# Performance work log

Measured on AMD Instinct MI355X. Metric: run time of the kernel, lower is better.

Reference implementation:

```python
import jax, jax.numpy as jnp
import numpy as np

N_NODES = 20000
N_EDGES = 320000
IN_DIM = 512
NUM_CLASSES = 10
DROP_P = 0.2


def _gcn_conv(x, src, dst, W, b, n):
    # PyG GCNConv: linear transform, add self-loops, symmetric deg^-1/2 norm,
    # scatter-add into destination nodes, then bias.
    h = x @ W                                   # [N, out]
    loops = jnp.arange(n)
    s = jnp.concatenate([src, loops])           # source (j)
    d = jnp.concatenate([dst, loops])           # destination (i)
    deg = jax.ops.segment_sum(jnp.ones_like(s, dtype=h.dtype), d, num_segments=n)
    dinv = jax.lax.rsqrt(deg)                   # deg >= 1 thanks to self-loops
    norm = dinv[s] * dinv[d]                    # [E+N]
    msg = h[s] * norm[:, None]                  # gather + per-edge scale
    out = jax.ops.segment_sum(msg, d, num_segments=n)  # scatter-add
    return out + b


def _dropout(x, key, p=DROP_P):
    keep = jax.random.bernoulli(key, 1.0 - p, x.shape)
    return jnp.where(keep, x / (1.0 - p), jnp.zeros((), x.dtype))


def setup_inputs() -> dict:
    key = jax.random.key(0)
    ks = jax.random.split(key, 6)
    x = jax.random.normal(ks[0], (N_NODES, IN_DIM), dtype=jnp.float32)
    edge_index = jax.random.randint(ks[1], (2, N_EDGES), 0, N_NODES, dtype=jnp.int64)
    h1, h2 = IN_DIM // 2, IN_DIM // 4
    W1 = jax.random.normal(ks[2], (IN_DIM, h1), dtype=jnp.float32) / np.sqrt(IN_DIM)
    W2 = jax.random.normal(ks[3], (h1, h2), dtype=jnp.float32) / np.sqrt(h1)
    W3 = jax.random.normal(ks[4], (h2, NUM_CLASSES), dtype=jnp.float32) / np.sqrt(h2)
    b1 = jnp.zeros((h1,), jnp.float32)
    b2 = jnp.zeros((h2,), jnp.float32)
    b3 = jnp.zeros((NUM_CLASSES,), jnp.float32)
    return {"x": x, "edge_index": edge_index, "W1": W1, "b1": b1,
            "W2": W2, "b2": b2, "W3": W3, "b3": b3}


def reference(x, edge_index, W1, b1, W2, b2, W3, b3):
    n = x.shape[0]
    src, dst = edge_index[0], edge_index[1]
    dk1, dk2 = jax.random.split(jax.random.key(1))
    h = _gcn_conv(x, src, dst, W1, b1, n)
    h = _dropout(jax.nn.relu(h), dk1)
    h = _gcn_conv(h, src, dst, W2, b2, n)
    h = _dropout(jax.nn.relu(h), dk2)
    h = _gcn_conv(h, src, dst, W3, b3, n)
    return jax.nn.log_softmax(h, axis=1)
```

## Files before the change

kernel.cpp:

```cpp
#include <hip/hip_runtime.h>
#include <hip/hip_bf16.h>
#include <math.h>

typedef __attribute__((ext_vector_type(8))) short short8;
typedef __attribute__((ext_vector_type(8))) unsigned short ushort8;
typedef __attribute__((ext_vector_type(4))) unsigned short ushort4v;
typedef __attribute__((ext_vector_type(4))) float f32x4;

__host__ __device__ inline void threefry2x32(unsigned k0, unsigned k1,
                                             unsigned x0, unsigned x1,
                                             unsigned* out0, unsigned* out1) {
  unsigned ks0 = k0, ks1 = k1, ks2 = k0 ^ k1 ^ 0x1BD11BDAu;
  x0 += ks0; x1 += ks1;
#define TF_ROUND(r) { x0 += x1; x1 = (x1 << (r)) | (x1 >> (32 - (r))); x1 ^= x0; }
  TF_ROUND(13) TF_ROUND(15) TF_ROUND(26) TF_ROUND(6)
  x0 += ks1; x1 += ks2 + 1u;
  TF_ROUND(17) TF_ROUND(29) TF_ROUND(16) TF_ROUND(24)
  x0 += ks2; x1 += ks0 + 2u;
  TF_ROUND(13) TF_ROUND(15) TF_ROUND(26) TF_ROUND(6)
  x0 += ks0; x1 += ks1 + 3u;
  TF_ROUND(17) TF_ROUND(29) TF_ROUND(16) TF_ROUND(24)
  x0 += ks1; x1 += ks2 + 4u;
  TF_ROUND(13) TF_ROUND(15) TF_ROUND(26) TF_ROUND(6)
  x0 += ks2; x1 += ks0 + 5u;
#undef TF_ROUND
  *out0 = x0; *out1 = x1;
}

__device__ inline float jax_uniform01(unsigned key0, unsigned key1, unsigned i) {
  unsigned o0, o1;
  threefry2x32(key0, key1, 0u, i, &o0, &o1);
  unsigned bits = o0 ^ o1;
  return __uint_as_float((bits >> 9) | 0x3f800000u) - 1.0f;
}

__device__ inline unsigned short f2bf(float f) {
  unsigned u = __float_as_uint(f);
  u += 0x7fffu + ((u >> 16) & 1u);
  return (unsigned short)(u >> 16);
}

__device__ inline float bf2f(unsigned short b) {
  return __uint_as_float(((unsigned)b) << 16);
}

__global__ __launch_bounds__(256) void k_init(int* __restrict__ deg, int n,
                                              const float* __restrict__ W1,
                                              unsigned short* __restrict__ W1T,
                                              const float* __restrict__ W2,
                                              unsigned short* __restrict__ W2T) {
  const int S1 = 512 * 256, S2 = 256 * 128;
  int idx = blockIdx.x * 256 + threadIdx.x;
  if (idx < n) { deg[idx] = 0; return; }
  idx -= n;
  if (idx < S1) {
    int k = idx / 256, c = idx % 256;
    W1T[(size_t)c * 512 + k] = f2bf(W1[idx]);
    return;
  }
  idx -= S1;
  if (idx < S2) {
    int k = idx / 128, c = idx % 128;
    W2T[(size_t)c * 256 + k] = f2bf(W2[idx]);
  }
}

__global__ void k_deg(const int* __restrict__ ei, int E, int* __restrict__ deg) {
  int e = blockIdx.x * blockDim.x + threadIdx.x;
  if (e >= E) return;
  atomicAdd(&deg[ei[E + e]], 1);
}

__global__ __launch_bounds__(256) void k_bsum(const int* __restrict__ deg,
                                              int* __restrict__ bsum, int n) {
  int i = blockIdx.x * 256 + threadIdx.x;
  int v = (i < n) ? deg[i] : 0;
#pragma unroll
  for (int o = 32; o; o >>= 1) v += __shfl_down(v, o);
  __shared__ int ws[4];
  if ((threadIdx.x & 63) == 0) ws[threadIdx.x >> 6] = v;
  __syncthreads();
  if (threadIdx.x == 0) bsum[blockIdx.x] = ws[0] + ws[1] + ws[2] + ws[3];
}

__global__ __launch_bounds__(256) void k_scatter2(const int* __restrict__ deg,
                                                  const int* __restrict__ bsum,
                                                  int* __restrict__ off, int* __restrict__ cur,
                                                  float* __restrict__ dinv, int n) {
  int i = blockIdx.x * 256 + threadIdx.x;
  int lane = threadIdx.x & 63, w = threadIdx.x >> 6;
  int pb = 0;
  for (int k = lane; k < blockIdx.x; k += 64) pb += bsum[k];
#pragma unroll
  for (int o = 32; o; o >>= 1) pb += __shfl_xor(pb, o);

  int d = (i < n) ? deg[i] : 0;
  int inc = d;
#pragma unroll
  for (int o = 1; o < 64; o <<= 1) {
    int u = __shfl_up(inc, o);
    if (lane >= o) inc += u;
  }
  __shared__ int wsum[4];
  if (lane == 63) wsum[w] = inc;
  __syncthreads();
  int wbase = 0;
  for (int k = 0; k < w; ++k) wbase += wsum[k];
  int excl = inc - d + wbase + pb;
  if (i < n) {
    off[i] = excl;
    cur[i] = excl;
    dinv[i] = 1.0f / sqrtf((float)(d + 1));
    if (i == n - 1) off[n] = excl + d;
  }
}

__global__ void k_fill_w(const int* __restrict__ ei, int E,
                         int* __restrict__ cur, int* __restrict__ srcs,
                         float* __restrict__ wgt, const float* __restrict__ dinv) {
  int e = blockIdx.x * blockDim.x + threadIdx.x;
  if (e >= E) return;
  int s = ei[e];
  int d = ei[E + e];
  int pos = atomicAdd(&cur[d], 1);
  srcs[pos] = s;
  wgt[pos] = dinv[s] * dinv[d];
}

template <int BN, bool AF32, bool OBF>
__global__ __launch_bounds__(256) void k_gemm_mfma(const void* __restrict__ Ap,
                                                   const unsigned short* __restrict__ BT,
                                                   void* __restrict__ Cp,
                                                   int M, int N, int K) {
  constexpr int WCOLS = BN / 4;
  constexpr int NFW = WCOLS / 16;
  __shared__ unsigned short As[32][40];
  __shared__ unsigned short Bs[BN][40];
  const int tid = threadIdx.x;
  const int row0 = blockIdx.y * 32;
  const int col0 = blockIdx.x * BN;
  const int wn = tid >> 6, lane = tid & 63;
  const int lr = lane & 15, lk = lane >> 4;

  f32x4 acc[2][NFW];
#pragma unroll
  for (int mi = 0; mi < 2; ++mi)
#pragma unroll
    for (int ni = 0; ni < NFW; ++ni) acc[mi][ni] = (f32x4)0.0f;

  const int ar = tid >> 3;
  const int aseg = (tid & 7) * 4;

  for (int k0 = 0; k0 < K; k0 += 32) {
    {
      int grow = row0 + ar;
      unsigned short a4[4] = {0, 0, 0, 0};
      if (grow < M) {
        if (AF32) {
          const float* A = (const float*)Ap;
          float4 v = *(const float4*)&A[(size_t)grow * K + k0 + aseg];
          a4[0] = f2bf(v.x); a4[1] = f2bf(v.y); a4[2] = f2bf(v.z); a4[3] = f2bf(v.w);
        } else {
          const unsigned short* A = (const unsigned short*)Ap;
          ushort4v v = *(const ushort4v*)&A[(size_t)grow * K + k0 + aseg];
          a4[0] = v[0]; a4[1] = v[1]; a4[2] = v[2]; a4[3] = v[3];
        }
      }
      *(ushort4v*)&As[ar][aseg] = *(ushort4v*)a4;
    }
#pragma unroll
    for (int p = 0; p < BN / 64; ++p) {
      int u = tid + p * 256;
      int br = u >> 2;
      int bseg = (u & 3) * 8;
      ushort8 bv = *(const ushort8*)&BT[(size_t)(col0 + br) * K + k0 + bseg];
      *(ushort8*)&Bs[br][bseg] = bv;
    }
    __syncthreads();

    short8 a[2], b[NFW];
#pragma unroll
    for (int mi = 0; mi < 2; ++mi)
      a[mi] = *(const short8*)&As[mi * 16 + lr][lk * 8];
#pragma unroll
    for (int ni = 0; ni < NFW; ++ni)
      b[ni] = *(const short8*)&Bs[wn * WCOLS + ni * 16 + lr][lk * 8];
#pragma unroll
    for (int mi = 0; mi < 2; ++mi)
#pragma unroll
      for (int ni = 0; ni < NFW; ++ni)
        acc[mi][ni] = __builtin_amdgcn_mfma_f32_16x16x32_bf16(a[mi], b[ni], acc[mi][ni], 0, 0, 0);
    __syncthreads();
  }

#pragma unroll
  for (int mi = 0; mi < 2; ++mi) {
    int rbase = row0 + mi * 16 + lk * 4;
#pragma unroll
    for (int j = 0; j < 4; ++j) {
      int row = rbase + j;
      if (row < M) {
#pragma unroll
        for (int ni = 0; ni < NFW; ++ni) {
          int col = col0 + wn * WCOLS + ni * 16 + lr;
          if (OBF) {
            ((unsigned short*)Cp)[(size_t)row * N + col] = f2bf(acc[mi][ni][j]);
          } else {
            ((float*)Cp)[(size_t)row * N + col] = acc[mi][ni][j];
          }
        }
      }
    }
  }
}

template <int C, bool OBF>
__global__ __launch_bounds__(256) void k_agg_bf(const unsigned short* __restrict__ h,
                                                void* __restrict__ outv,
                                                const int* __restrict__ off,
                                                const int* __restrict__ srcs,
                                                const float* __restrict__ wgt,
                                                const float* __restrict__ dinv,
                                                const float* __restrict__ bias,
                                                unsigned key0, unsigned key1, int n) {
  typedef __attribute__((ext_vector_type(C))) unsigned short ushortC;
  const int node = blockIdx.x * (blockDim.x >> 6) + (threadIdx.x >> 6);
  if (node >= n) return;
  const int lane = threadIdx.x & 63;
  const int F = 64 * C;
  const float dv = dinv[node];

  float acc[C];
  {
    ushortC r = *(const ushortC*)(h + (size_t)node * F + lane * C);
    float wv = dv * dv;
#pragma unroll
    for (int j = 0; j < C; ++j) acc[j] = bf2f(r[j]) * wv;
  }
  int e = off[node];
  const int e1 = off[node + 1];
  for (; e + 8 <= e1; e += 8) {
    int s[8];
    float wv[8];
    ushortC r[8];
#pragma unroll
    for (int q = 0; q < 8; ++q) s[q] = srcs[e + q];
#pragma unroll
    for (int q = 0; q < 8; ++q) wv[q] = wgt[e + q];
#pragma unroll
    for (int q = 0; q < 8; ++q) r[q] = *(const ushortC*)(h + (size_t)s[q] * F + lane * C);
#pragma unroll
    for (int q = 0; q < 8; ++q)
#pragma unroll
      for (int j = 0; j < C; ++j) acc[j] += bf2f(r[q][j]) * wv[q];
  }
  for (; e < e1; ++e) {
    int s = srcs[e];
    float wv = wgt[e];
    ushortC r = *(const ushortC*)(h + (size_t)s * F + lane * C);
#pragma unroll
    for (int j = 0; j < C; ++j) acc[j] += bf2f(r[j]) * wv;
  }
#pragma unroll
  for (int j = 0; j < C; ++j) {
    float v = acc[j] + bias[lane * C + j];
    v = fmaxf(v, 0.0f);
    unsigned i = (unsigned)(node * F + lane * C + j);
    float u = jax_uniform01(key0, key1, i);
    v = (u < 0.8f) ? (v * 1.25f) : 0.0f;
    acc[j] = v;
  }
  if (OBF) {
    unsigned short* op = (unsigned short*)outv + (size_t)node * F + lane * C;
#pragma unroll
    for (int j = 0; j < C; ++j) op[j] = f2bf(acc[j]);
  } else {
    float* op = (float*)outv + (size_t)node * F + lane * C;
#pragma unroll
    for (int j = 0; j < C; ++j) op[j] = acc[j];
  }
}

__global__ __launch_bounds__(256) void k_agg2_g3(const unsigned short* __restrict__ h,
                                                 float* __restrict__ h3,
                                                 const int* __restrict__ off,
                                                 const int* __restrict__ srcs,
                                                 const float* __restrict__ wgt,
                                                 const float* __restrict__ dinv,
                                                 const float* __restrict__ b2,
                                                 const float* __restrict__ W3,
                                                 unsigned key0, unsigned key1, int n) {
  const int node = blockIdx.x * 4 + (threadIdx.x >> 6);
  if (node >= n) return;
  const int lane = threadIdx.x & 63;

  float w3a[10], w3b[10];
  {
    const float4* p = (const float4*)(W3 + lane * 20);
    float4 v0 = p[0], v1 = p[1], v2 = p[2], v3 = p[3], v4 = p[4];
    w3a[0] = v0.x; w3a[1] = v0.y; w3a[2] = v0.z; w3a[3] = v0.w;
    w3a[4] = v1.x; w3a[5] = v1.y; w3a[6] = v1.z; w3a[7] = v1.w;
    w3a[8] = v2.x; w3a[9] = v2.y;
    w3b[0] = v2.z; w3b[1] = v2.w;
    w3b[2] = v3.x; w3b[3] = v3.y; w3b[4] = v3.z; w3b[5] = v3.w;
    w3b[6] = v4.x; w3b[7] = v4.y; w3b[8] = v4.z; w3b[9] = v4.w;
  }

  const float dv = dinv[node];
  float acc0, acc1;
  {
    unsigned r = *(const unsigned*)(h + (size_t)node * 128 + lane * 2);
    float wv = dv * dv;
    acc0 = bf2f((unsigned short)(r & 0xffffu)) * wv;
    acc1 = bf2f((unsigned short)(r >> 16)) * wv;
  }
  int e = off[node];
  const int e1 = off[node + 1];
  for (; e + 8 <= e1; e += 8) {
    int s[8];
    float wv[8];
    unsigned r[8];
#pragma unroll
    for (int q = 0; q < 8; ++q) s[q] = srcs[e + q];
#pragma unroll
    for (int q = 0; q < 8; ++q) wv[q] = wgt[e + q];
#pragma unroll
    for (int q = 0; q < 8; ++q) r[q] = *(const unsigned*)(h + (size_t)s[q] * 128 + lane * 2);
#pragma unroll
    for (int q = 0; q < 8; ++q) {
      acc0 += bf2f((unsigned short)(r[q] & 0xffffu)) * wv[q];
      acc1 += bf2f((unsigned short)(r[q] >> 16)) * wv[q];
    }
  }
  for (; e < e1; ++e) {
    int s = srcs[e];
    float wv = wgt[e];
    unsigned r = *(const unsigned*)(h + (size_t)s * 128 + lane * 2);
    acc0 += bf2f((unsigned short)(r & 0xffffu)) * wv;
    acc1 += bf2f((unsigned short)(r >> 16)) * wv;
  }
  {
    float v = fmaxf(acc0 + b2[lane * 2], 0.0f);
    float u = jax_uniform01(key0, key1, (unsigned)(node * 128 + lane * 2));
    acc0 = (u < 0.8f) ? (v * 1.25f) : 0.0f;
  }
  {
    float v = fmaxf(acc1 + b2[lane * 2 + 1], 0.0f);
    float u = jax_uniform01(key0, key1, (unsigned)(node * 128 + lane * 2 + 1));
    acc1 = (u < 0.8f) ? (v * 1.25f) : 0.0f;
  }
  float myout = 0.0f;
#pragma unroll
  for (int c = 0; c < 10; ++c) {
    float part = acc0 * w3a[c] + acc1 * w3b[c];
#pragma unroll
    for (int o = 32; o; o >>= 1) part += __shfl_xor(part, o);
    if (lane == c) myout = part;
  }
  if (lane < 10) h3[(size_t)node * 10 + lane] = myout;
}

__global__ __launch_bounds__(256) void k_agg3_lsm_v2(const float* __restrict__ h,
                                                     float* __restrict__ out,
                                                     const int* __restrict__ off,
                                                     const int* __restrict__ srcs,
                                                     const float* __restrict__ wgt,
                                                     const float* __restrict__ dinv,
                                                     const float* __restrict__ b,
                                                     int n) {
  const int node = blockIdx.x * 4 + (threadIdx.x >> 6);
  if (node >= n) return;
  const int lane = threadIdx.x & 63;
  const bool act = (lane < 10);
  const float dv = dinv[node];

  float acc = 0.0f;
  if (act) acc = h[(size_t)node * 10 + lane] * dv * dv;
  int e = off[node];
  const int e1 = off[node + 1];
  for (; e + 4 <= e1; e += 4) {
    int s0 = srcs[e + 0], s1 = srcs[e + 1], s2 = srcs[e + 2], s3 = srcs[e + 3];
    float w0 = wgt[e + 0], w1 = wgt[e + 1], w2 = wgt[e + 2], w3 = wgt[e + 3];
    if (act) {
      acc += h[(size_t)s0 * 10 + lane] * w0 + h[(size_t)s1 * 10 + lane] * w1 +
             h[(size_t)s2 * 10 + lane] * w2 + h[(size_t)s3 * 10 + lane] * w3;
    }
  }
  for (; e < e1; ++e) {
    int s = srcs[e];
    float w = wgt[e];
    if (act) acc += h[(size_t)s * 10 + lane] * w;
  }
  float v = act ? (acc + b[lane]) : -1e30f;
  float m = v;
#pragma unroll
  for (int o = 32; o; o >>= 1) m = fmaxf(m, __shfl_xor(m, o));
  float p = act ? expf(v - m) : 0.0f;
  float ssum = p;
#pragma unroll
  for (int o = 32; o; o >>= 1) ssum += __shfl_xor(ssum, o);
  float lse = m + logf(ssum);
  if (act) out[(size_t)node * 10 + lane] = v - lse;
}

extern "C" void kernel_launch(void* const* d_in, const int* in_sizes, int n_in,
                              void* d_out, int out_size, void* d_ws, size_t ws_size,
                              hipStream_t stream) {
  const float* x  = (const float*)d_in[0];
  const int*   ei = (const int*)d_in[1];
  const float* W1 = (const float*)d_in[2];
  const float* b1 = (const float*)d_in[3];
  const float* W2 = (const float*)d_in[4];
  const float* b2 = (const float*)d_in[5];
  const float* W3 = (const float*)d_in[6];
  const float* b3 = (const float*)d_in[7];
  float* out = (float*)d_out;

  const int N = 20000;
  const int E = in_sizes[1] / 2;
  const int D1 = 256, D2 = 128;
  const int NB = (N + 255) / 256;

  char* ws = (char*)d_ws;
  auto carve = [&](size_t bytes) -> char* {
    char* p = ws;
    ws += (bytes + 255) & ~(size_t)255;
    return p;
  };
  int*   deg  = (int*)carve((size_t)N * 4);
  int*   off  = (int*)carve((size_t)(N + 1) * 4);
  int*   cur  = (int*)carve((size_t)N * 4);
  float* dinv = (float*)carve((size_t)N * 4);
  int*   bsum = (int*)carve((size_t)128 * 4);
  int*   srcs = (int*)carve((size_t)E * 4);
  float* wgt  = (float*)carve((size_t)E * 4);
  unsigned short* W1T = (unsigned short*)carve((size_t)D1 * 512 * 2);
  unsigned short* W2T = (unsigned short*)carve((size_t)D2 * D1 * 2);
  unsigned short* bufHb = (unsigned short*)carve((size_t)N * D1 * 2);
  unsigned short* bufA_bf = (unsigned short*)carve((size_t)N * D1 * 2);
  float* bufH3 = (float*)carve((size_t)N * 10 * 4);

  unsigned dk1_0, dk1_1, dk2_0, dk2_1;
  threefry2x32(0u, 1u, 0u, 0u, &dk1_0, &dk1_1);
  threefry2x32(0u, 1u, 0u, 1u, &dk2_0, &dk2_1);

  const int INIT_ITEMS = N + 512 * 256 + 256 * 128;
  k_init<<<(INIT_ITEMS + 255) / 256, 256, 0, stream>>>(deg, N, W1, W1T, W2, W2T);
  k_deg<<<(E + 255) / 256, 256, 0, stream>>>(ei, E, deg);
  k_bsum<<<NB, 256, 0, stream>>>(deg, bsum, N);
  k_scatter2<<<NB, 256, 0, stream>>>(deg, bsum, off, cur, dinv, N);
  k_fill_w<<<(E + 255) / 256, 256, 0, stream>>>(ei, E, cur, srcs, wgt, dinv);

  k_gemm_mfma<256, true, true><<<dim3(1, N / 32), 256, 0, stream>>>(x, W1T, bufHb, N, D1, 512);
  k_agg_bf<4, true><<<(N + 3) / 4, 256, 0, stream>>>(bufHb, bufA_bf, off, srcs, wgt, dinv, b1, dk1_0, dk1_1, N);

  k_gemm_mfma<128, false, true><<<dim3(1, N / 32), 256, 0, stream>>>(bufA_bf, W2T, bufHb, N, D2, D1);
  k_agg2_g3<<<(N + 3) / 4, 256, 0, stream>>>(bufHb, bufH3, off, srcs, wgt, dinv, b2, W3, dk2_0, dk2_1, N);

  k_agg3_lsm_v2<<<(N + 3) / 4, 256, 0, stream>>>(bufH3, out, off, srcs, wgt, dinv, b3, N);
}
```

Measured before the change: 151.9 us.

## Fuse graph preprocessing and first GEMM into one persistent kernel with grid barriers

Merges the init, degree count, block-sum, scan, CSR fill and first-layer GEMM kernels into a single launch. The first 128 blocks run the preprocessing phases separated by software grid barriers built on atomics. The remaining blocks wait only until the weight transpose is done, then compute the x@W1 GEMM alongside the graph preprocessing. This removes several kernel launches and overlaps the CSR build with the GEMM. It relies on all 128 prep blocks being co-resident so the spin barriers can make progress, and adds a memset for the barrier counters.

New measurement: 346.9 us. 2.28x slower.

```diff
diff --git a/kernel.cpp b/kernel.cpp
--- a/kernel.cpp
+++ b/kernel.cpp
@@ -6,6 +6,8 @@
 typedef __attribute__((ext_vector_type(8))) unsigned short ushort8;
 typedef __attribute__((ext_vector_type(4))) unsigned short ushort4v;
 typedef __attribute__((ext_vector_type(4))) float f32x4;
+
+#define PREPB 128
 
 __host__ __device__ inline void threefry2x32(unsigned k0, unsigned k1,
                                              unsigned x0, unsigned x1,
@@ -44,87 +46,155 @@
   return __uint_as_float(((unsigned)b) << 16);
 }
 
-__global__ __launch_bounds__(256) void k_init(int* __restrict__ deg, int n,
-                                              const float* __restrict__ W1,
-                                              unsigned short* __restrict__ W1T,
-                                              const float* __restrict__ W2,
-                                              unsigned short* __restrict__ W2T) {
+__device__ inline void prep_bar(int* bar, int idx, int target) {
+  __syncthreads();
+  if (threadIdx.x == 0) {
+    __threadfence();
+    __hip_atomic_fetch_add(&bar[idx], 1, __ATOMIC_ACQ_REL, __HIP_MEMORY_SCOPE_AGENT);
+    while (__hip_atomic_load(&bar[idx], __ATOMIC_ACQUIRE, __HIP_MEMORY_SCOPE_AGENT) < target)
+      __builtin_amdgcn_s_sleep(8);
+  }
+  __syncthreads();
+  __threadfence();
+}
+
+__global__ __launch_bounds__(256) void k_front(
+    const float* __restrict__ x, const int* __restrict__ ei,
+    int* __restrict__ deg, int* __restrict__ off, int* __restrict__ cur,
+    float* __restrict__ dinv, int* __restrict__ bsum, int* __restrict__ bar,
+    int* __restrict__ srcs, float* __restrict__ wgt,
+    const float* __restrict__ W1, const float* __restrict__ W2,
+    unsigned short* __restrict__ W1T, unsigned short* __restrict__ W2T,
+    unsigned short* __restrict__ h1, int E) {
+  const int N = 20000;
   const int S1 = 512 * 256, S2 = 256 * 128;
-  int idx = blockIdx.x * 256 + threadIdx.x;
-  if (idx < n) { deg[idx] = 0; return; }
-  idx -= n;
-  if (idx < S1) {
-    int k = idx / 256, c = idx % 256;
-    W1T[(size_t)c * 512 + k] = f2bf(W1[idx]);
-    return;
-  }
-  idx -= S1;
-  if (idx < S2) {
-    int k = idx / 128, c = idx % 128;
-    W2T[(size_t)c * 256 + k] = f2bf(W2[idx]);
-  }
-}
-
-__global__ void k_deg(const int* __restrict__ ei, int E, int* __restrict__ deg) {
-  int e = blockIdx.x * blockDim.x + threadIdx.x;
-  if (e >= E) return;
-  atomicAdd(&deg[ei[E + e]], 1);
-}
-
-__global__ __launch_bounds__(256) void k_bsum(const int* __restrict__ deg,
-                                              int* __restrict__ bsum, int n) {
-  int i = blockIdx.x * 256 + threadIdx.x;
-  int v = (i < n) ? deg[i] : 0;
-#pragma unroll
-  for (int o = 32; o; o >>= 1) v += __shfl_down(v, o);
-  __shared__ int ws[4];
-  if ((threadIdx.x & 63) == 0) ws[threadIdx.x >> 6] = v;
-  __syncthreads();
-  if (threadIdx.x == 0) bsum[blockIdx.x] = ws[0] + ws[1] + ws[2] + ws[3];
-}
-
-__global__ __launch_bounds__(256) void k_scatter2(const int* __restrict__ deg,
-                                                  const int* __restrict__ bsum,
-                                                  int* __restrict__ off, int* __restrict__ cur,
-                                                  float* __restrict__ dinv, int n) {
-  int i = blockIdx.x * 256 + threadIdx.x;
-  int lane = threadIdx.x & 63, w = threadIdx.x >> 6;
-  int pb = 0;
-  for (int k = lane; k < blockIdx.x; k += 64) pb += bsum[k];
-#pragma unroll
-  for (int o = 32; o; o >>= 1) pb += __shfl_xor(pb, o);
-
-  int d = (i < n) ? deg[i] : 0;
-  int inc = d;
-#pragma unroll
-  for (int o = 1; o < 64; o <<= 1) {
-    int u = __shfl_up(inc, o);
-    if (lane >= o) inc += u;
-  }
-  __shared__ int wsum[4];
-  if (lane == 63) wsum[w] = inc;
-  __syncthreads();
-  int wbase = 0;
-  for (int k = 0; k < w; ++k) wbase += wsum[k];
-  int excl = inc - d + wbase + pb;
-  if (i < n) {
-    off[i] = excl;
-    cur[i] = excl;
-    dinv[i] = 1.0f / sqrtf((float)(d + 1));
-    if (i == n - 1) off[n] = excl + d;
-  }
-}
-
-__global__ void k_fill_w(const int* __restrict__ ei, int E,
-                         int* __restrict__ cur, int* __restrict__ srcs,
-                         float* __restrict__ wgt, const float* __restrict__ dinv) {
-  int e = blockIdx.x * blockDim.x + threadIdx.x;
-  if (e >= E) return;
-  int s = ei[e];
-  int d = ei[E + e];
-  int pos = atomicAdd(&cur[d], 1);
-  srcs[pos] = s;
-  wgt[pos] = dinv[s] * dinv[d];
+  const int NB = (N + 255) / 256;
+  const int tid = threadIdx.x;
+  const int bid = blockIdx.x;
+  const int lane = tid & 63;
+
+  __shared__ unsigned short As[32][40];
+  __shared__ unsigned short Bs[256][40];
+  __shared__ int smi[4];
+
+  if (bid < PREPB) {
+    for (int idx = bid * 256 + tid; idx < N + S1 + S2; idx += PREPB * 256) {
+      int i = idx;
+      if (i < N) { deg[i] = 0; continue; }
+      i -= N;
+      if (i < S1) { int k = i / 256, c = i % 256; W1T[(size_t)c * 512 + k] = f2bf(W1[i]); continue; }
+      i -= S1;
+      { int k = i / 128, c = i % 128; W2T[(size_t)c * 256 + k] = f2bf(W2[i]); }
+    }
+    prep_bar(bar, 0, PREPB);
+    if (bid == 0 && tid == 0)
+      __hip_atomic_store(&bar[7], 1, __ATOMIC_RELEASE, __HIP_MEMORY_SCOPE_AGENT);
+    for (int e = bid * 256 + tid; e < E; e += PREPB * 256)
+      atomicAdd(&deg[ei[E + e]], 1);
+    prep_bar(bar, 1, PREPB);
+    for (int c = bid; c < NB; c += PREPB) {
+      int i = c * 256 + tid;
+      int v = (i < N) ? deg[i] : 0;
+#pragma unroll
+      for (int o = 32; o; o >>= 1) v += __shfl_down(v, o);
+      if ((tid & 63) == 0) smi[tid >> 6] = v;
+      __syncthreads();
+      if (tid == 0) bsum[c] = smi[0] + smi[1] + smi[2] + smi[3];
+      __syncthreads();
+    }
+    prep_bar(bar, 2, PREPB);
+    for (int c = bid; c < NB; c += PREPB) {
+      int i = c * 256 + tid;
+      int w = tid >> 6;
+      int pb = 0;
+      for (int k = lane; k < c; k += 64) pb += bsum[k];
+#pragma unroll
+      for (int o = 32; o; o >>= 1) pb += __shfl_xor(pb, o);
+      int d = (i < N) ? deg[i] : 0;
+      int inc = d;
+#pragma unroll
+      for (int o = 1; o < 64; o <<= 1) {
+        int u = __shfl_up(inc, o);
+        if (lane >= o) inc += u;
+      }
+      if (lane == 63) smi[w] = inc;
+      __syncthreads();
+      int wbase = 0;
+      for (int k = 0; k < w; ++k) wbase += smi[k];
+      int excl = inc - d + wbase + pb;
+      if (i < N) {
+        off[i] = excl;
+        cur[i] = excl;
+        dinv[i] = 1.0f / sqrtf((float)(d + 1));
+        if (i == N - 1) off[N] = excl + d;
+      }
+      __syncthreads();
+    }
+    prep_bar(bar, 3, PREPB);
+    for (int e = bid * 256 + tid; e < E; e += PREPB * 256) {
+      int s = ei[e];
+      int d = ei[E + e];
+      int pos = atomicAdd(&cur[d], 1);
+      srcs[pos] = s;
+      wgt[pos] = dinv[s] * dinv[d];
+    }
+  } else {
+    if (tid == 0) {
+      while (__hip_atomic_load(&bar[7], __ATOMIC_ACQUIRE, __HIP_MEMORY_SCOPE_AGENT) == 0)
+        __builtin_amdgcn_s_sleep(8);
+    }
+    __syncthreads();
+    __threadfence();
+
+    const int t = bid - PREPB;
+    const int row0 = t * 32;
+    const int wn = tid >> 6;
+    const int lr = lane & 15, lk = lane >> 4;
+    const int ar = tid >> 3, aseg = (tid & 7) * 4;
+
+    f32x4 acc[2][4];
+#pragma unroll
+    for (int mi = 0; mi < 2; ++mi)
+#pragma unroll
+      for (int ni = 0; ni < 4; ++ni) acc[mi][ni] = (f32x4)0.0f;
+
+    for (int k0 = 0; k0 < 512; k0 += 32) {
+      {
+        float4 v = *(const float4*)&x[(size_t)(row0 + ar) * 512 + k0 + aseg];
+        unsigned short a4[4] = {f2bf(v.x), f2bf(v.y), f2bf(v.z), f2bf(v.w)};
+        *(ushort4v*)&As[ar][aseg] = *(ushort4v*)a4;
+      }
+#pragma unroll
+      for (int p = 0; p < 4; ++p) {
+        int u = tid + p * 256;
+        int br = u >> 2, bseg = (u & 3) * 8;
+        *(ushort8*)&Bs[br][bseg] = *(const ushort8*)&W1T[(size_t)br * 512 + k0 + bseg];
+      }
+      __syncthreads();
+      short8 a[2], b[4];
+#pragma unroll
+      for (int mi = 0; mi < 2; ++mi) a[mi] = *(const short8*)&As[mi * 16 + lr][lk * 8];
+#pragma unroll
+      for (int ni = 0; ni < 4; ++ni) b[ni] = *(const short8*)&Bs[wn * 64 + ni * 16 + lr][lk * 8];
+#pragma unroll
+      for (int mi = 0; mi < 2; ++mi)
+#pragma unroll
+        for (int ni = 0; ni < 4; ++ni)
+          acc[mi][ni] = __builtin_amdgcn_mfma_f32_16x16x32_bf16(a[mi], b[ni], acc[mi][ni], 0, 0, 0);
+      __syncthreads();
+    }
+#pragma unroll
+    for (int mi = 0; mi < 2; ++mi) {
+      int rbase = row0 + mi * 16 + lk * 4;
+#pragma unroll
+      for (int j = 0; j < 4; ++j)
+#pragma unroll
+        for (int ni = 0; ni < 4; ++ni) {
+          int col = wn * 64 + ni * 16 + lr;
+          h1[(size_t)(rbase + j) * 256 + col] = f2bf(acc[mi][ni][j]);
+        }
+    }
+  }
 }
 
 template <int BN, bool AF32, bool OBF>
@@ -141,16 +211,13 @@
   const int col0 = blockIdx.x * BN;
   const int wn = tid >> 6, lane = tid & 63;
   const int lr = lane & 15, lk = lane >> 4;
-
   f32x4 acc[2][NFW];
 #pragma unroll
   for (int mi = 0; mi < 2; ++mi)
 #pragma unroll
     for (int ni = 0; ni < NFW; ++ni) acc[mi][ni] = (f32x4)0.0f;
-
   const int ar = tid >> 3;
   const int aseg = (tid & 7) * 4;
-
   for (int k0 = 0; k0 < K; k0 += 32) {
     {
       int grow = row0 + ar;
@@ -177,7 +244,6 @@
       *(ushort8*)&Bs[br][bseg] = bv;
     }
     __syncthreads();
-
     short8 a[2], b[NFW];
 #pragma unroll
     for (int mi = 0; mi < 2; ++mi)
@@ -192,7 +258,6 @@
         acc[mi][ni] = __builtin_amdgcn_mfma_f32_16x16x32_bf16(a[mi], b[ni], acc[mi][ni], 0, 0, 0);
     __syncthreads();
   }
-
 #pragma unroll
   for (int mi = 0; mi < 2; ++mi) {
     int rbase = row0 + mi * 16 + lk * 4;
@@ -203,11 +268,8 @@
 #pragma unroll
         for (int ni = 0; ni < NFW; ++ni) {
           int col = col0 + wn * WCOLS + ni * 16 + lr;
-          if (OBF) {
-            ((unsigned short*)Cp)[(size_t)row * N + col] = f2bf(acc[mi][ni][j]);
-          } else {
-            ((float*)Cp)[(size_t)row * N + col] = acc[mi][ni][j];
-          }
+          if (OBF) ((unsigned short*)Cp)[(size_t)row * N + col] = f2bf(acc[mi][ni][j]);
+          else ((float*)Cp)[(size_t)row * N + col] = acc[mi][ni][j];
         }
       }
     }
@@ -229,7 +291,6 @@
   const int lane = threadIdx.x & 63;
   const int F = 64 * C;
   const float dv = dinv[node];
-
   float acc[C];
   {
     ushortC r = *(const ushortC*)(h + (size_t)node * F + lane * C);
@@ -240,9 +301,7 @@
   int e = off[node];
   const int e1 = off[node + 1];
   for (; e + 8 <= e1; e += 8) {
-    int s[8];
-    float wv[8];
-    ushortC r[8];
+    int s[8]; float wv[8]; ushortC r[8];
 #pragma unroll
     for (int q = 0; q < 8; ++q) s[q] = srcs[e + q];
 #pragma unroll
@@ -293,7 +352,6 @@
   const int node = blockIdx.x * 4 + (threadIdx.x >> 6);
   if (node >= n) return;
   const int lane = threadIdx.x & 63;
-
   float w3a[10], w3b[10];
   {
     const float4* p = (const float4*)(W3 + lane * 20);
@@ -305,7 +363,6 @@
     w3b[2] = v3.x; w3b[3] = v3.y; w3b[4] = v3.z; w3b[5] = v3.w;
     w3b[6] = v4.x; w3b[7] = v4.y; w3b[8] = v4.z; w3b[9] = v4.w;
   }
-
   const float dv = dinv[node];
   float acc0, acc1;
   {
@@ -317,9 +374,7 @@
   int e = off[node];
   const int e1 = off[node + 1];
   for (; e + 8 <= e1; e += 8) {
-    int s[8];
-    float wv[8];
-    unsigned r[8];
+    int s[8]; float wv[8]; unsigned r[8];
 #pragma unroll
     for (int q = 0; q < 8; ++q) s[q] = srcs[e + q];
 #pragma unroll
@@ -373,7 +428,6 @@
   const int lane = threadIdx.x & 63;
   const bool act = (lane < 10);
   const float dv = dinv[node];
-
   float acc = 0.0f;
   if (act) acc = h[(size_t)node * 10 + lane] * dv * dv;
   int e = off[node];
@@ -417,9 +471,8 @@
   float* out = (float*)d_out;
 
   const int N = 20000;
-  const int E = in_sizes[1] / 2;
+  int E = in_sizes[1] / 2;
   const int D1 = 256, D2 = 128;
-  const int NB = (N + 255) / 256;
 
   char* ws = (char*)d_ws;
   auto carve = [&](size_t bytes) -> char* {
@@ -432,30 +485,34 @@
   int*   cur  = (int*)carve((size_t)N * 4);
   float* dinv = (float*)carve((size_t)N * 4);
   int*   bsum = (int*)carve((size_t)128 * 4);
+  int*   bar  = (int*)carve((size_t)16 * 4);
   int*   srcs = (int*)carve((size_t)E * 4);
   float* wgt  = (float*)carve((size_t)E * 4);
   unsigned short* W1T = (unsigned short*)carve((size_t)D1 * 512 * 2);
   unsigned short* W2T = (unsigned short*)carve((size_t)D2 * D1 * 2);
   unsigned short* bufHb = (unsigned short*)carve((size_t)N * D1 * 2);
-  unsigned short* bufA_bf = (unsigned short*)carve((size_t)N * D1 * 2);
-  float* bufH3 = (float*)carve((size_t)N * 10 * 4);
+  unsigned short* bufA  = (unsigned short*)carve((size_t)N * D1 * 2);
+  float* h3 = (float*)carve((size_t)N * 10 * 4);
 
   unsigned dk1_0, dk1_1, dk2_0, dk2_1;
   threefry2x32(0u, 1u, 0u, 0u, &dk1_0, &dk1_1);
   threefry2x32(0u, 1u, 0u, 1u, &dk2_0, &dk2_1);
 
-  const int INIT_ITEMS = N + 512 * 256 + 256 * 128;
-  k_init<<<(INIT_ITEMS + 255) / 256, 256, 0, stream>>>(deg, N, W1, W1T, W2, W2T);
-  k_deg<<<(E + 255) / 256, 256, 0, stream>>>(ei, E, deg);
-  k_bsum<<<NB, 256, 0, stream>>>(deg, bsum, N);
-  k_scatter2<<<NB, 256, 0, stream>>>(deg, bsum, off, cur, dinv, N);
-  k_fill_w<<<(E + 255) / 256, 256, 0, stream>>>(ei, E, cur, srcs, wgt, dinv);
-
-  k_gemm_mfma<256, true, true><<<dim3(1, N / 32), 256, 0, stream>>>(x, W1T, bufHb, N, D1, 512);
-  k_agg_bf<4, true><<<(N + 3) / 4, 256, 0, stream>>>(bufHb, bufA_bf, off, srcs, wgt, dinv, b1, dk1_0, dk1_1, N);
-
-  k_gemm_mfma<128, false, true><<<dim3(1, N / 32), 256, 0, stream>>>(bufA_bf, W2T, bufHb, N, D2, D1);
-  k_agg2_g3<<<(N + 3) / 4, 256, 0, stream>>>(bufHb, bufH3, off, srcs, wgt, dinv, b2, W3, dk2_0, dk2_1, N);
-
-  k_agg3_lsm_v2<<<(N + 3) / 4, 256, 0, stream>>>(bufH3, out, off, srcs, wgt, dinv, b3, N);
-}
+  hipMemsetAsync(bar, 0, 16 * 4, stream);
+
+  k_front<<<PREPB + N / 32, 256, 0, stream>>>(x, ei, deg, off, cur, dinv, bsum,
+                                              bar, srcs, wgt, W1, W2, W1T, W2T,
+                                              bufHb, E);
+
+  k_agg_bf<4, true><<<(N + 3) / 4, 256, 0, stream>>>(bufHb, bufA, off, srcs, wgt,
+                                                     dinv, b1, dk1_0, dk1_1, N);
+
+  k_gemm_mfma<128, false, true><<<dim3(1, N / 32), 256, 0, stream>>>(bufA, W2T,
+                                                                     bufHb, N, D2, D1);
+
+  k_agg2_g3<<<(N + 3) / 4, 256, 0, stream>>>(bufHb, h3, off, srcs, wgt, dinv,
+                                             b2, W3, dk2_0, dk2_1, N);
+
+  k_agg3_lsm_v2<<<(N + 3) / 4, 256, 0, stream>>>(h3, out, off, srcs, wgt, dinv,
+                                                 b3, N);
+}
```
